# Optimization experiments

Measured on AMD Instinct MI355X. Metric: run time of the kernel, lower is better.

The kernel has to match this reference:

```python
import jax, jax.numpy as jnp
import numpy as np

NT, NS, NH, NG = 365, 2048, 64, 128
PI = 3.1415  # constant used by the original code (not math.pi)


def setup_inputs() -> dict:
    key = jax.random.key(0)
    kP, kE, kTm, kdT, kxc, kW, kb = jax.random.split(key, 7)
    # Physically plausible forcings: positive precip/evap, T1 < T2 always
    P = jax.random.uniform(kP, (NT, NS)) * 20.0
    E = jax.random.uniform(kE, (NT, NS)) * 5.0
    Tm = jax.random.normal(kTm, (NT, NS)) * 10.0
    dT = jax.random.uniform(kdT, (NT, NS)) * 10.0 + 1.0
    T1 = Tm - dT / 2
    T2 = Tm + dT / 2
    x = jnp.stack([P, E, T1, T2], axis=-1)  # [nt, ns, 4]
    xc = jax.random.normal(kxc, (NS, NG))
    W = jax.random.normal(kW, (NH * 8 + 1, NG)) * 0.05  # fc weight
    b = jax.random.normal(kb, (NH * 8 + 1,)) * 0.05     # fc bias
    return {"x": x, "xc": xc, "W": W, "b": b}


def reference(x, xc, W, b):
    nh = (W.shape[0] - 1) // 8
    P, E, T1, T2 = x[..., 0], x[..., 1], x[..., 2], x[..., 3]  # each [nt, ns]
    Ta = (T1 + T2) / 2
    mask1 = T1 >= 0
    mask0 = T2 <= 0
    # nan-safe arccos argument: value is overwritten by the masks anyway
    arg = jnp.where(mask1 | mask0, 0.0, (T1 + T2) / (T2 - T1))
    rP = 1 - jnp.arccos(arg) / PI
    rP = jnp.where(mask1, 1.0, rP)
    rP = jnp.where(mask0, 0.0, rP)
    Ps = (1 - rP) * P  # snow
    Pl = rP * P        # liquid

    w = xc @ W.T + b  # [ns, nh*8+1]
    gm = jnp.exp(w[:, :nh]) + 1
    ge = jax.nn.sigmoid(w[:, nh:2 * nh]) * 2
    k0 = jax.nn.sigmoid(w[:, 3 * nh:4 * nh])
    k1 = jax.nn.sigmoid(w[:, 4 * nh:5 * nh])
    k2 = jax.nn.sigmoid(w[:, 5 * nh:6 * nh])
    gl = jnp.exp(w[:, 6 * nh:7 * nh])
    ga = jax.nn.softmax(w[:, 4 * nh:5 * nh], axis=1)  # dropout in eval = id
    qb = jax.nn.relu(w[:, -1]) / nh  # [ns]
    kb = jax.nn.sigmoid(w[:, 7 * nh:8 * nh]) / 10
    vi = jax.nn.sigmoid(w[:, 8 * nh:8 * nh + 1])  # (ns, 1) — faithful to source slice

    ns = P.shape[1]
    z = jnp.zeros((ns, nh), dtype=x.dtype)

    def step(carry, inp):
        S0, H0, H1, H2 = carry
        ps, pl, e, ta = inp  # each [ns]
        S = S0 + ps[:, None]
        Sm = jnp.minimum(S0, jax.nn.relu(ta[:, None] * gm))
        G1 = jax.nn.relu(H1 + Sm + pl[:, None] * vi - e[:, None] * ge)
        G0 = jax.nn.relu(H0 + G1 - gl + pl[:, None] * (1 - vi))
        Q0 = G0 * k0
        Q1a = jnp.minimum(G1, gl) * k1
        Q1 = Q1a * (1 - kb)
        G2 = H2 + Q1a * kb
        Q2 = G2 * k2
        Y = jnp.sum((Q0 + Q1 + Q2 + qb[:, None]) * ga, axis=1)
        return (S - Sm, G0 - Q0, jnp.minimum(G1 - Q1a, gl), G2 - Q2), Y

    _, Yout = jax.lax.scan(step, (z, z, z, z), (Ps, Pl, E, Ta))
    return Yout  # [nt, ns]
```

## Files before the change

### kernel.cpp

```cpp
#include <hip/hip_runtime.h>
#include <math.h>

#define NT 365
#define NS 2048
#define NH 64
#define NG 128
#define NW 513
#define WSTR 520

__device__ __forceinline__ float sigmoidf_(float x) {
    return 1.0f / (1.0f + __expf(-x));
}

__global__ __launch_bounds__(256) void prep_kernel(const float* __restrict__ xc,
                                                   const float* __restrict__ Wm,
                                                   const float* __restrict__ bv,
                                                   float* __restrict__ w,
                                                   const float* __restrict__ x,
                                                   float* __restrict__ f) {
    __shared__ float xcs[64][132];
    __shared__ float Wsh[64][132];
    const int tid = threadIdx.x;

    if (blockIdx.x >= 256) {
        int i = (blockIdx.x - 256) * 256 + tid;
        float4 v = ((const float4*)x)[i];
        float P = v.x, E = v.y, T1 = v.z, T2 = v.w;
        float Ta = 0.5f * (T1 + T2);
        float rP;
        if (T2 <= 0.0f)       rP = 0.0f;
        else if (T1 >= 0.0f)  rP = 1.0f;
        else                  rP = 1.0f - acosf((T1 + T2) / (T2 - T1)) * (1.0f / 3.1415f);
        float Ps = (1.0f - rP) * P;
        float Pl = rP * P;
        ((float4*)f)[i] = make_float4(Ps, Pl, E, fmaxf(Ta, 0.0f));
        return;
    }

    const int sTile = (blockIdx.x >> 3) * 64;
    const int by = blockIdx.x & 7;
    const int jt = (by >= 2) ? by + 1 : by;
    const int jTile = jt * 64;

    for (int i = 0; i < 8; i++) {
        int f4  = tid + i * 256;
        int row = f4 >> 5;
        int c4  = (f4 & 31) * 4;
        float4 v = ((const float4*)(xc + (size_t)(sTile + row) * NG))[f4 & 31];
        xcs[row][c4] = v.x; xcs[row][c4 + 1] = v.y; xcs[row][c4 + 2] = v.z; xcs[row][c4 + 3] = v.w;
        int jr = jTile + row;
        float4 wv = make_float4(0.f, 0.f, 0.f, 0.f);
        if (jr < NW) wv = ((const float4*)(Wm + (size_t)jr * NG))[f4 & 31];
        Wsh[row][c4] = wv.x; Wsh[row][c4 + 1] = wv.y; Wsh[row][c4 + 2] = wv.z; Wsh[row][c4 + 3] = wv.w;
    }
    __syncthreads();

    const int tx = tid & 15, ty = tid >> 4;
    float acc[4][4] = {};
#pragma unroll 4
    for (int k = 0; k < 128; k++) {
        float a0 = xcs[ty][k], a1 = xcs[ty + 16][k], a2 = xcs[ty + 32][k], a3 = xcs[ty + 48][k];
        float b0 = Wsh[tx][k], b1 = Wsh[tx + 16][k], b2 = Wsh[tx + 32][k], b3 = Wsh[tx + 48][k];
        acc[0][0] += a0 * b0; acc[0][1] += a0 * b1; acc[0][2] += a0 * b2; acc[0][3] += a0 * b3;
        acc[1][0] += a1 * b0; acc[1][1] += a1 * b1; acc[1][2] += a1 * b2; acc[1][3] += a1 * b3;
        acc[2][0] += a2 * b0; acc[2][1] += a2 * b1; acc[2][2] += a2 * b2; acc[2][3] += a2 * b3;
        acc[3][0] += a3 * b0; acc[3][1] += a3 * b1; acc[3][2] += a3 * b2; acc[3][3] += a3 * b3;
    }
#pragma unroll
    for (int i = 0; i < 4; i++) {
        int s = sTile + ty + 16 * i;
#pragma unroll
        for (int j = 0; j < 4; j++) {
            int jj = jTile + tx + 16 * j;
            if (jj < NW) w[(size_t)s * WSTR + jj] = acc[i][j] + bv[jj];
        }
    }
}

template <bool PRE>
__global__ __launch_bounds__(256) void scan_kernel(const float* __restrict__ fx,
                                                   const float* __restrict__ w,
                                                   float* __restrict__ Y) {
    __shared__ float ybuf[4][64][33];
    const int wave = threadIdx.x >> 6;
    const int lane = threadIdx.x & 63;
    const int s = blockIdx.x * 4 + wave;
    const float* wr = w + (size_t)s * WSTR;

    float gm = __expf(wr[lane]) + 1.0f;
    float geN = -2.0f * sigmoidf_(wr[64 + lane]);
    float k0 = sigmoidf_(wr[192 + lane]);
    float w4 = wr[256 + lane];
    float k1 = sigmoidf_(w4);
    float k2 = sigmoidf_(wr[320 + lane]);
    float gl = __expf(wr[384 + lane]);
    float kb = sigmoidf_(wr[448 + lane]) * 0.1f;
    float wl = wr[512];
    float qb = fmaxf(wl, 0.0f) * (1.0f / (float)NH);
    float vi = sigmoidf_(wl);

    float m = w4;
#pragma unroll
    for (int off = 32; off; off >>= 1) m = fmaxf(m, __shfl_xor(m, off));
    float ex = __expf(w4 - m);
    float sum = ex;
#pragma unroll
    for (int off = 32; off; off >>= 1) sum += __shfl_xor(sum, off);
    float ga = ex / sum;

    float c0   = k0 * ga;
    float c1   = k1 * (1.0f - kb) * ga;
    float c2   = k2 * ga;
    float k0c  = 1.0f - k0;
    float k2c  = 1.0f - k2;
    float glN  = -gl;
    float viC  = 1.0f - vi;
    float k1kb = k1 * kb;
    float k1N  = -k1;

    float S0 = 0.f, H0 = 0.f, H1 = 0.f, H2 = 0.f;

    const char* fb = (const char*)fx;
    unsigned off0 = (unsigned)s * 16u;
    asm volatile("" : "+v"(off0));
    unsigned offs[8];
    float4 vbuf[8];
#pragma unroll
    for (int b = 0; b < 8; b++) {
        offs[b] = off0 + (unsigned)(b * NS * 16);
        vbuf[b] = *(const float4*)(fb + offs[b]);
        offs[b] += 8u * NS * 16u;
    }

    float* wp = &ybuf[wave][lane][0];
    const float* rp = &ybuf[wave][(lane >> 5) << 5][lane & 31];

#define STEP_COMP(vv, tl)                                                      \
    {                                                                          \
        float Ps, Pl, E, TaR;                                                  \
        if (PRE) { Ps = vv.x; Pl = vv.y; E = vv.z; TaR = vv.w; }               \
        else {                                                                 \
            float P = vv.x; E = vv.y;                                          \
            float T1 = vv.z, T2 = vv.w;                                        \
            float Ta = 0.5f * (T1 + T2);                                       \
            float rP;                                                          \
            if (T2 <= 0.0f)      rP = 0.0f;                                    \
            else if (T1 >= 0.0f) rP = 1.0f;                                    \
            else rP = 1.0f - acosf((T1 + T2) / (T2 - T1)) * (1.0f / 3.1415f);  \
            Ps = (1.0f - rP) * P; Pl = rP * P; TaR = fmaxf(Ta, 0.0f);          \
        }                                                                      \
        float S   = S0 + Ps;                                                   \
        float Sm  = fminf(S0, gm * TaR);                                       \
        S0 = S - Sm;                                                           \
        float G1  = fmaxf(H1 + Sm + fmaf(E, geN, Pl * vi), 0.0f);              \
        float G0  = fmaxf(H0 + G1 + fmaf(Pl, viC, glN), 0.0f);                 \
        float m1  = fminf(G1, gl);                                             \
        float G2  = fmaf(m1, k1kb, H2);                                        \
        wp[tl] = fmaf(G0, c0, fmaf(m1, c1, G2 * c2));                          \
        H0 = G0 * k0c;                                                         \
        H1 = fminf(fmaf(m1, k1N, G1), gl);                                     \
        H2 = G2 * k2c;                                                         \
    }

#define TRRED(t0)                                                              \
    {                                                                          \
        float a0 = 0.f, a1 = 0.f, a2 = 0.f, a3 = 0.f;                          \
        _Pragma("unroll")                                                      \
        for (int j = 0; j < 32; j += 4) {                                      \
            a0 += rp[(size_t)j * 33];                                          \
            a1 += rp[(size_t)(j + 1) * 33];                                    \
            a2 += rp[(size_t)(j + 2) * 33];                                    \
            a3 += rp[(size_t)(j + 3) * 33];                                    \
        }                                                                      \
        float part = (a0 + a1) + (a2 + a3);                                    \
        float full = part + __shfl_xor(part, 32);                              \
        int t = (t0) + (lane & 31);                                            \
        if (lane < 32 && t < NT) Y[(size_t)t * NS + s] = full + qb;            \
    }

    for (int sb = 0; sb < 11; ++sb) {
#pragma unroll
        for (int tl = 0; tl < 32; ++tl) {
            float4 v = vbuf[tl & 7];
            vbuf[tl & 7] = *(const float4*)(fb + offs[tl & 7]);
            offs[tl & 7] += 8u * NS * 16u;
            STEP_COMP(v, tl);
        }
        TRRED(sb * 32);
    }
    {
        const int t0 = 352;
#pragma unroll
        for (int tl = 0; tl < 32; ++tl) {
            float4 v = vbuf[tl & 7];
            int tn = t0 + tl + 8; tn = tn < NT ? tn : NT - 1;
            vbuf[tl & 7] = *(const float4*)(fb + (off0 + (unsigned)(tn * NS * 16)));
            STEP_COMP(v, tl);
        }
        TRRED(t0);
    }
#undef STEP_COMP
#undef TRRED
}

extern "C" void kernel_launch(void* const* d_in, const int* in_sizes, int n_in,
                              void* d_out, int out_size, void* d_ws, size_t ws_size,
                              hipStream_t stream) {
    const float* x  = (const float*)d_in[0];
    const float* xc = (const float*)d_in[1];
    const float* Wm = (const float*)d_in[2];
    const float* bv = (const float*)d_in[3];
    float* out = (float*)d_out;

    float* wbuf = (float*)d_ws;
    size_t wbytes = (size_t)NS * WSTR * sizeof(float);
    float* fbuf = (float*)((char*)d_ws + wbytes);
    size_t need = wbytes + (size_t)NT * NS * 4 * sizeof(float);

    if (ws_size >= need) {
        prep_kernel<<<256 + (NT * NS) / 256, 256, 0, stream>>>(xc, Wm, bv, wbuf, x, fbuf);
        scan_kernel<true><<<NS / 4, 256, 0, stream>>>(fbuf, wbuf, out);
    } else {
        prep_kernel<<<256, 256, 0, stream>>>(xc, Wm, bv, wbuf, x, fbuf);
        scan_kernel<false><<<NS / 4, 256, 0, stream>>>(x, wbuf, out);
    }
}
```

Baseline: 106.9 us.

## Transpose precomputed forcing buffer to site-major layout for contiguous scan loads

The forcing preprocessing now writes its output in a site-major layout (each site's 365 timesteps stored contiguously, padded to 368), and the scan kernel reads it with small per-site offsets instead of strides of NS*16 bytes. The aim is to turn scattered time-strided loads into sequential per-thread streams and to simplify address arithmetic. The cost is that the prep kernel now does strided reads of x and uses far fewer blocks (128 instead of ~2920), so the transposition may be slower. Per-wave loads in the scan also become uncoalesced across lanes, since neighbouring lanes are now 368*16 bytes apart.

```diff
diff --git a/kernel.cpp b/kernel.cpp
--- a/kernel.cpp
+++ b/kernel.cpp
@@ -7,6 +7,7 @@
 #define NG 128
 #define NW 513
 #define WSTR 520
+#define FTR 368
 
 __device__ __forceinline__ float sigmoidf_(float x) {
     return 1.0f / (1.0f + __expf(-x));
@@ -23,17 +24,24 @@
     const int tid = threadIdx.x;
 
     if (blockIdx.x >= 256) {
-        int i = (blockIdx.x - 256) * 256 + tid;
-        float4 v = ((const float4*)x)[i];
-        float P = v.x, E = v.y, T1 = v.z, T2 = v.w;
-        float Ta = 0.5f * (T1 + T2);
-        float rP;
-        if (T2 <= 0.0f)       rP = 0.0f;
-        else if (T1 >= 0.0f)  rP = 1.0f;
-        else                  rP = 1.0f - acosf((T1 + T2) / (T2 - T1)) * (1.0f / 3.1415f);
-        float Ps = (1.0f - rP) * P;
-        float Pl = rP * P;
-        ((float4*)f)[i] = make_float4(Ps, Pl, E, fmaxf(Ta, 0.0f));
+        const int b = blockIdx.x - 256;
+        const int site16 = tid >> 4;
+        const int phase  = tid & 15;
+        const int s = b * 16 + site16;
+        const float4* xp = (const float4*)x;
+        float4* fpo = (float4*)f + (size_t)s * FTR;
+        for (int tt = phase; tt < NT; tt += 16) {
+            float4 v = xp[(size_t)tt * NS + s];
+            float P = v.x, E = v.y, T1 = v.z, T2 = v.w;
+            float Ta = 0.5f * (T1 + T2);
+            float rP;
+            if (T2 <= 0.0f)       rP = 0.0f;
+            else if (T1 >= 0.0f)  rP = 1.0f;
+            else                  rP = 1.0f - acosf((T1 + T2) / (T2 - T1)) * (1.0f / 3.1415f);
+            float Ps = (1.0f - rP) * P;
+            float Pl = rP * P;
+            fpo[tt] = make_float4(Ps, Pl, E, fmaxf(Ta, 0.0f));
+        }
         return;
     }
 
@@ -120,16 +128,15 @@
 
     float S0 = 0.f, H0 = 0.f, H1 = 0.f, H2 = 0.f;
 
-    const char* fb = (const char*)fx;
-    unsigned off0 = (unsigned)s * 16u;
-    asm volatile("" : "+v"(off0));
-    unsigned offs[8];
+    const char* fB = (const char*)fx;
+    unsigned voff = PRE ? (unsigned)s * (FTR * 16u) : (unsigned)s * 16u;
+    asm volatile("" : "+v"(voff));
+
     float4 vbuf[8];
 #pragma unroll
     for (int b = 0; b < 8; b++) {
-        offs[b] = off0 + (unsigned)(b * NS * 16);
-        vbuf[b] = *(const float4*)(fb + offs[b]);
-        offs[b] += 8u * NS * 16u;
+        if (PRE) vbuf[b] = *(const float4*)(fB + voff + b * 16);
+        else     vbuf[b] = *(const float4*)(fB + (size_t)b * (NS * 16) + voff);
     }
 
     float* wp = &ybuf[wave][lane][0];
@@ -179,22 +186,29 @@
     }
 
     for (int sb = 0; sb < 11; ++sb) {
+        const char* fs = fB + sb * (32 * 16);
 #pragma unroll
         for (int tl = 0; tl < 32; ++tl) {
             float4 v = vbuf[tl & 7];
-            vbuf[tl & 7] = *(const float4*)(fb + offs[tl & 7]);
-            offs[tl & 7] += 8u * NS * 16u;
+            if (PRE)
+                vbuf[tl & 7] = *(const float4*)(fs + voff + (tl + 8) * 16);
+            else
+                vbuf[tl & 7] = *(const float4*)(fB + (size_t)(sb * 32 + tl + 8) * (NS * 16) + voff);
             STEP_COMP(v, tl);
         }
         TRRED(sb * 32);
     }
     {
         const int t0 = 352;
+        const char* fs = fB + 11 * (32 * 16);
 #pragma unroll
         for (int tl = 0; tl < 32; ++tl) {
             float4 v = vbuf[tl & 7];
-            int tn = t0 + tl + 8; tn = tn < NT ? tn : NT - 1;
-            vbuf[tl & 7] = *(const float4*)(fb + (off0 + (unsigned)(tn * NS * 16)));
+            const int rel = (tl + 8 > 12) ? 12 : (tl + 8);
+            if (PRE)
+                vbuf[tl & 7] = *(const float4*)(fs + voff + rel * 16);
+            else
+                vbuf[tl & 7] = *(const float4*)(fB + (size_t)(t0 + rel) * (NS * 16) + voff);
             STEP_COMP(v, tl);
         }
         TRRED(t0);
@@ -215,10 +229,10 @@
     float* wbuf = (float*)d_ws;
     size_t wbytes = (size_t)NS * WSTR * sizeof(float);
     float* fbuf = (float*)((char*)d_ws + wbytes);
-    size_t need = wbytes + (size_t)NT * NS * 4 * sizeof(float);
+    size_t need = wbytes + (size_t)NS * FTR * 16;
 
     if (ws_size >= need) {
-        prep_kernel<<<256 + (NT * NS) / 256, 256, 0, stream>>>(xc, Wm, bv, wbuf, x, fbuf);
+        prep_kernel<<<256 + NS / 16, 256, 0, stream>>>(xc, Wm, bv, wbuf, x, fbuf);
         scan_kernel<true><<<NS / 4, 256, 0, stream>>>(fbuf, wbuf, out);
     } else {
         prep_kernel<<<256, 256, 0, stream>>>(xc, Wm, bv, wbuf, x, fbuf);
```

New measurement: 110.2 us. +3.1%, slower.
